# Optimization experiments

Measured on AMD Instinct MI355X. Metric: run time of the kernel, lower is better.

Reference implementation:

```python
import jax, jax.numpy as jnp
import numpy as np

N_NODES = 50000
N_EDGES = 600000
N_RELS = 19
D_IN = 128
D_HID = 64
D_OUT = 2


def setup_inputs() -> dict:
    key = jax.random.key(0)
    ks = jax.random.split(key, 10)
    feat = jax.random.normal(ks[0], (N_NODES, D_IN), dtype=jnp.float32)
    src = jax.random.randint(ks[1], (N_EDGES,), 0, N_NODES)
    dst = jax.random.randint(ks[2], (N_EDGES,), 0, N_NODES)
    etype = jax.random.randint(ks[3], (N_EDGES,), 0, N_RELS)
    s1 = 1.0 / np.sqrt(D_IN)
    s2 = 1.0 / np.sqrt(D_HID)
    W1 = jax.random.normal(ks[4], (N_RELS, D_IN, D_HID), dtype=jnp.float32) * s1
    loop1 = jax.random.normal(ks[5], (D_IN, D_HID), dtype=jnp.float32) * s1
    b1 = jnp.zeros((D_HID,), dtype=jnp.float32)
    W2 = jax.random.normal(ks[6], (N_RELS, D_HID, D_OUT), dtype=jnp.float32) * s2
    loop2 = jax.random.normal(ks[7], (D_HID, D_OUT), dtype=jnp.float32) * s2
    b2 = jnp.zeros((D_OUT,), dtype=jnp.float32)
    return {"feat": feat, "W1": W1, "loop1": loop1, "b1": b1,
            "W2": W2, "loop2": loop2, "b2": b2,
            "src": src, "dst": dst, "etype": etype}


def _rel_graph_conv(h, W, loop_w, bias, src, dst, etype, activation):
    # Per-relation transform of all nodes: [N, R, O]; then gather per edge.
    # (num_rels * out_feat is small, so this is cheaper than gathering W per edge.)
    transformed = jnp.einsum('nd,rdo->nro', h, W)
    msg = transformed[src, etype]                      # [E, O] edge messages
    agg = jax.ops.segment_sum(msg, dst, num_segments=h.shape[0])  # scatter-add
    out = agg + h @ loop_w + bias                      # self-loop + bias
    if activation is not None:
        out = activation(out)
    return out


def reference(feat, W1, loop1, b1, W2, loop2, b2, src, dst, etype):
    h = _rel_graph_conv(feat, W1, loop1, b1, src, dst, etype, jax.nn.relu)
    h = _rel_graph_conv(h, W2, loop2, b2, src, dst, etype, None)
    return h
```

## Files before the change

kernel.cpp:

```cpp
#include <hip/hip_runtime.h>

#define N_NODES 50000
#define N_EDGES 600000
#define N_RELS  19
#define D_IN    128
#define D_HID   64
#define D_OUT   2
#define EDGE_TILES ((N_EDGES + 127) / 128 + N_RELS)
#define SL_BLOCKS  ((N_NODES + 63) / 64)
#define PREP_ELEMS (N_RELS * D_HID * D_IN + 48 * 64 + D_HID * D_IN)
#define PREP_BLOCKS ((PREP_ELEMS + 255) / 256)

typedef unsigned short u16;
typedef unsigned int   u32;
typedef __attribute__((ext_vector_type(8))) short sfrag;
typedef __attribute__((ext_vector_type(4))) float f32x4;

__device__ __forceinline__ u16 f2bf(float f){
  union { float f; u32 i; } v; v.f = f;
  u32 r = v.i + 0x7fffu + ((v.i >> 16) & 1u);
  return (u16)(r >> 16);
}
__device__ __forceinline__ float bf2f(u16 u){
  union { u32 i; float f; } v; v.i = ((u32)u) << 16; return v.f;
}

__global__ __launch_bounds__(256) void k_fused_pre(const float* __restrict__ feat,
                                                   u16* __restrict__ featb,
                                                   const int* __restrict__ et,
                                                   const int* __restrict__ dst,
                                                   int* __restrict__ hist_rel,
                                                   int* __restrict__ hist_dst){
  int i = blockIdx.x * 256 + threadIdx.x;
  float2 f = ((const float2*)feat)[i];
  ((u32*)featb)[i] = (u32)f2bf(f.x) | ((u32)f2bf(f.y) << 16);
  if (blockIdx.x < (N_EDGES + 255) / 256) {
    __shared__ int lh[N_RELS];
    int tid = threadIdx.x;
    if (tid < N_RELS) lh[tid] = 0;
    __syncthreads();
    int e = blockIdx.x * 256 + tid;
    if (e < N_EDGES) {
      atomicAdd(&lh[et[e]], 1);
      atomicAdd(&hist_dst[dst[e]], 1);
    }
    __syncthreads();
    if (tid < N_RELS && lh[tid]) atomicAdd(&hist_rel[tid], lh[tid]);
  }
}

__global__ __launch_bounds__(256) void k_alloc_scan(
    const int* __restrict__ hist_dst, int* __restrict__ dstart,
    int* __restrict__ cur_dst, int* __restrict__ gcnt,
    const int* __restrict__ hist_rel, int* __restrict__ offs,
    int* __restrict__ toff, int* __restrict__ cur_rel,
    const float* __restrict__ W1, const float* __restrict__ loop1,
    const float* __restrict__ W2, u16* __restrict__ W1Tb,
    u16* __restrict__ loop1Tb, u16* __restrict__ W2allT){
  if (blockIdx.x >= 197) {
    int idx = (blockIdx.x - 197) * 256 + threadIdx.x;
    const int T1 = N_RELS * D_HID * D_IN;
    const int T2c = T1 + 48 * 64;
    const int T3 = T2c + D_HID * D_IN;
    if (idx < T1) {
      int r = idx / (D_HID * D_IN);
      int t = idx - r * (D_HID * D_IN);
      int j = t >> 7, d = t & 127;
      W1Tb[idx] = f2bf(W1[(r * D_IN + d) * D_HID + j]);
    } else if (idx < T2c) {
      int k2 = idx - T1;
      int n = k2 >> 6, k = k2 & 63;
      float val = 0.f;
      if (n < N_RELS * D_OUT) {
        int r = n >> 1, o = n & 1;
        val = W2[(r * D_HID + k) * D_OUT + o];
      }
      W2allT[k2] = f2bf(val);
    } else if (idx < T3) {
      int k2 = idx - T2c;
      int j = k2 >> 7, d = k2 & 127;
      loop1Tb[k2] = f2bf(loop1[d * D_HID + j]);
    }
    return;
  }
  if (blockIdx.x == 196) {
    if (threadIdx.x == 0) {
      int acc = 0, tacc = 0;
      offs[0] = 0; toff[0] = 0;
      for (int r = 0; r < N_RELS; ++r) {
        cur_rel[r] = acc;
        int c = hist_rel[r];
        acc += c;                offs[r + 1] = acc;
        tacc += (c + 127) >> 7;  toff[r + 1] = tacc;
      }
    }
    return;
  }
  __shared__ int wbase[4];
  int tid = threadIdx.x, lane = tid & 63, wv = tid >> 6;
  int n = blockIdx.x * 256 + tid;
  int v = (n < N_NODES) ? hist_dst[n] : 0;
  int x = v;
  #pragma unroll
  for (int o = 1; o < 64; o <<= 1) { int u = __shfl_up(x, o); if (lane >= o) x += u; }
  if (lane == 63) wbase[wv] = atomicAdd(gcnt, x);
  __syncthreads();
  int start = wbase[wv] + x - v;
  if (n < N_NODES) { dstart[n] = start; cur_dst[n] = start; }
}

__global__ __launch_bounds__(256) void k_scatter_rel(const int* __restrict__ et,
                                                     int* __restrict__ cursor,
                                                     int* __restrict__ perm){
  __shared__ int lh[N_RELS], base[N_RELS];
  int tid = threadIdx.x;
  if (tid < N_RELS) lh[tid] = 0;
  __syncthreads();
  int e = blockIdx.x * 256 + tid;
  int r = 0, my = 0;
  bool valid = e < N_EDGES;
  if (valid) { r = et[e]; my = atomicAdd(&lh[r], 1); }
  __syncthreads();
  if (tid < N_RELS && lh[tid]) base[tid] = atomicAdd(&cursor[tid], lh[tid]);
  __syncthreads();
  if (valid) perm[base[r] + my] = e;
}

__global__ __launch_bounds__(256) void k_se1(
    const u16* __restrict__ featb, const u16* __restrict__ W1Tb,
    const u16* __restrict__ loop1Tb, const float* __restrict__ b1,
    const int* __restrict__ src, const int* __restrict__ dst,
    const int* __restrict__ perm, const int* __restrict__ offs,
    const int* __restrict__ toff, int* __restrict__ cur_dst,
    u16* __restrict__ msgbuf, float* __restrict__ agg1f){
  __shared__ __align__(16) u16 Bls[64][136];
  __shared__ __align__(16) u16 msg[128][72];
  __shared__ int posIds[128];
  int tid = threadIdx.x, lane = tid & 63, w = tid >> 6;
  int r16 = lane & 15, c4 = lane >> 4;

  if (blockIdx.x >= EDGE_TILES) {
    int base = (blockIdx.x - EDGE_TILES) * 64;
    { int j = tid >> 2, seg = tid & 3;
      const uint4* g = (const uint4*)(loop1Tb + j * 128) + seg * 4;
      uint4* d = (uint4*)&Bls[j][seg * 32];
      d[0] = g[0]; d[1] = g[1]; d[2] = g[2]; d[3] = g[3]; }
    int arow = base + w * 16 + r16; if (arow >= N_NODES) arow = N_NODES - 1;
    sfrag aF[4];
    #pragma unroll
    for (int kk = 0; kk < 4; ++kk)
      aF[kk] = *(const sfrag*)(featb + (size_t)arow * D_IN + kk * 32 + c4 * 8);
    __syncthreads();
    #pragma unroll
    for (int ct = 0; ct < 4; ++ct) {
      f32x4 acc = {0.f, 0.f, 0.f, 0.f};
      #pragma unroll
      for (int kk = 0; kk < 4; ++kk) {
        sfrag bF = *(const sfrag*)&Bls[ct * 16 + r16][kk * 32 + c4 * 8];
        acc = __builtin_amdgcn_mfma_f32_16x16x32_bf16(aF[kk], bF, acc, 0, 0, 0);
      }
      int col = ct * 16 + r16;
      float bias = b1[col];
      #pragma unroll
      for (int reg = 0; reg < 4; ++reg) {
        int orow = base + w * 16 + c4 * 4 + reg;
        if (orow < N_NODES) agg1f[(size_t)orow * D_HID + col] = acc[reg] + bias;
      }
    }
    return;
  }

  int b = blockIdx.x;
  unsigned long long mm = __ballot((lane < N_RELS) && (b >= toff[lane + 1]));
  int rel = __popcll(mm);
  if (rel >= N_RELS) return;
  int ts = offs[rel] + ((b - toff[rel]) << 7);
  int vc = offs[rel + 1] - ts; if (vc > 128) vc = 128;

  int myPos = -1;
  if (tid < 128 && tid < vc) {
    int e = perm[ts + tid];
    myPos = atomicAdd(&cur_dst[dst[e]], 1);
  }
  {
    int j = tid >> 2, seg = tid & 3;
    const uint4* g = (const uint4*)(W1Tb + ((size_t)rel * 64 + j) * 128) + seg * 4;
    uint4* d = (uint4*)&Bls[j][seg * 32];
    d[0] = g[0]; d[1] = g[1]; d[2] = g[2]; d[3] = g[3];
  }
  sfrag aF[2][4];
  #pragma unroll
  for (int mt = 0; mt < 2; ++mt) {
    int row = w * 32 + mt * 16 + r16;
    int rr = row < vc ? row : vc - 1;
    int s = src[perm[ts + rr]];
    const u16* ap = featb + (size_t)s * D_IN + c4 * 8;
    #pragma unroll
    for (int kk = 0; kk < 4; ++kk)
      aF[mt][kk] = *(const sfrag*)(ap + kk * 32);
  }
  __syncthreads();
  #pragma unroll
  for (int ct = 0; ct < 4; ++ct) {
    sfrag bF[4];
    #pragma unroll
    for (int kk = 0; kk < 4; ++kk)
      bF[kk] = *(const sfrag*)&Bls[ct * 16 + r16][kk * 32 + c4 * 8];
    #pragma unroll
    for (int mt = 0; mt < 2; ++mt) {
      f32x4 acc = {0.f, 0.f, 0.f, 0.f};
      #pragma unroll
      for (int kk = 0; kk < 4; ++kk)
        acc = __builtin_amdgcn_mfma_f32_16x16x32_bf16(aF[mt][kk], bF[kk], acc, 0, 0, 0);
      #pragma unroll
      for (int reg = 0; reg < 4; ++reg) {
        float v = acc[reg];
        float o = __shfl_xor(v, 1);
        float lo = (lane & 1) ? o : v;
        float hi = (lane & 1) ? v : o;
        u32 pk = (u32)f2bf(lo) | ((u32)f2bf(hi) << 16);
        if (!(lane & 1)) {
          int orow = w * 32 + mt * 16 + c4 * 4 + reg;
          *(u32*)&msg[orow][ct * 16 + r16] = pk;
        }
      }
    }
  }
  if (tid < 128) posIds[tid] = myPos;
  __syncthreads();
  { int row = tid >> 1, half = tid & 1;
    int pos = posIds[row];
    if (pos >= 0) {
      const uint4* mr = (const uint4*)&msg[row][half * 32];
      uint4* d = (uint4*)(msgbuf + (size_t)pos * D_HID + half * 32);
      d[0] = mr[0]; d[1] = mr[1]; d[2] = mr[2]; d[3] = mr[3];
    } }
}

__global__ __launch_bounds__(256) void k_agg_relu_self2(
    const u16* __restrict__ msgbuf, const int* __restrict__ dstart,
    const int* __restrict__ cnt, const float* __restrict__ agg1f,
    const float* __restrict__ loop2, const float* __restrict__ b2,
    u16* __restrict__ h1b, float* __restrict__ out){
  int wv = threadIdx.x >> 6, lane = threadIdx.x & 63;
  int n = blockIdx.x * 4 + wv;
  int s = dstart[n], epos = s + cnt[n];
  int h = lane >> 5, c = lane & 31;
  float a0 = 0.f, a1 = 0.f;
  for (int i = s + h; i < epos; i += 2) {
    u32 v = ((const u32*)msgbuf)[(size_t)i * 32 + c];
    a0 += bf2f((u16)(v & 0xffffu));
    a1 += bf2f((u16)(v >> 16));
  }
  a0 += __shfl_down(a0, 32);
  a1 += __shfl_down(a1, 32);
  float p0 = 0.f, p1 = 0.f;
  if (h == 0) {
    float2 sl = ((const float2*)(agg1f + (size_t)n * D_HID))[c];
    float v0 = a0 + sl.x, v1 = a1 + sl.y;
    v0 = v0 > 0.f ? v0 : 0.f;
    v1 = v1 > 0.f ? v1 : 0.f;
    ((u32*)h1b)[(size_t)n * 32 + c] = (u32)f2bf(v0) | ((u32)f2bf(v1) << 16);
    float2 w0 = ((const float2*)loop2)[2 * c];
    float2 w1 = ((const float2*)loop2)[2 * c + 1];
    p0 = v0 * w0.x + v1 * w1.x;
    p1 = v0 * w0.y + v1 * w1.y;
  }
  #pragma unroll
  for (int off = 16; off; off >>= 1) {
    p0 += __shfl_down(p0, off);
    p1 += __shfl_down(p1, off);
  }
  if (lane == 0) {
    out[n * 2]     = p0 + b2[0];
    out[n * 2 + 1] = p1 + b2[1];
  }
}

__global__ __launch_bounds__(256) void k_t2(
    const u16* __restrict__ h1b, const u16* __restrict__ W2allT,
    float* __restrict__ T2){
  __shared__ __align__(16) u16 Bls[48][72];
  int tid = threadIdx.x, lane = tid & 63, w = tid >> 6;
  int r16 = lane & 15, c4 = lane >> 4;
  for (int idx = tid; idx < 48 * 8; idx += 256) {
    int row = idx >> 3, q = idx & 7;
    ((uint4*)&Bls[row][0])[q] = ((const uint4*)W2allT)[idx];
  }
  int base = blockIdx.x * 64;
  int arow = base + w * 16 + r16; if (arow >= N_NODES) arow = N_NODES - 1;
  sfrag aF[2];
  #pragma unroll
  for (int kk = 0; kk < 2; ++kk)
    aF[kk] = *(const sfrag*)(h1b + (size_t)arow * D_HID + kk * 32 + c4 * 8);
  __syncthreads();
  #pragma unroll
  for (int ct = 0; ct < 3; ++ct) {
    f32x4 acc = {0.f, 0.f, 0.f, 0.f};
    #pragma unroll
    for (int kk = 0; kk < 2; ++kk) {
      sfrag bF = *(const sfrag*)&Bls[ct * 16 + r16][kk * 32 + c4 * 8];
      acc = __builtin_amdgcn_mfma_f32_16x16x32_bf16(aF[kk], bF, acc, 0, 0, 0);
    }
    int col = ct * 16 + r16;
    if (col < N_RELS * D_OUT) {
      #pragma unroll
      for (int reg = 0; reg < 4; ++reg) {
        int orow = base + w * 16 + c4 * 4 + reg;
        if (orow < N_NODES) T2[(size_t)orow * 40 + col] = acc[reg];
      }
    }
  }
}

__global__ __launch_bounds__(256) void k_edge2(
    const float* __restrict__ T2, const int* __restrict__ src,
    const int* __restrict__ dst, const int* __restrict__ et,
    float* __restrict__ out){
  int e = blockIdx.x * 256 + threadIdx.x;
  if (e >= N_EDGES) return;
  int s = src[e], d = dst[e], r = et[e];
  float2 v = *(const float2*)(T2 + (size_t)s * 40 + r * 2);
  atomicAdd(&out[d * 2],     v.x);
  atomicAdd(&out[d * 2 + 1], v.y);
}

extern "C" void kernel_launch(void* const* d_in, const int* in_sizes, int n_in,
                              void* d_out, int out_size, void* d_ws, size_t ws_size,
                              hipStream_t stream){
  const float* feat  = (const float*)d_in[0];
  const float* W1    = (const float*)d_in[1];
  const float* loop1 = (const float*)d_in[2];
  const float* b1    = (const float*)d_in[3];
  const float* W2    = (const float*)d_in[4];
  const float* loop2 = (const float*)d_in[5];
  const float* b2    = (const float*)d_in[6];
  const int* src     = (const int*)d_in[7];
  const int* dst     = (const int*)d_in[8];
  const int* et      = (const int*)d_in[9];
  float* out = (float*)d_out;

  char* w = (char*)d_ws;
  u16*   W1Tb     = (u16*)(w);
  u16*   W2allT   = (u16*)(w + 311296);
  u16*   loop1Tb  = (u16*)(w + 350208);
  int*   hist_rel = (int*)(w + 366592);
  int*   gcnt     = (int*)(w + 366720);
  int*   hist_dst = (int*)(w + 366848);
  int*   offs     = (int*)(w + 566848);
  int*   toff     = (int*)(w + 566976);
  int*   cur_rel  = (int*)(w + 567104);
  int*   dstart   = (int*)(w + 567232);
  int*   cur_dst  = (int*)(w + 767232);
  int*   perm     = (int*)(w + 967232);
  u16*   featb    = (u16*)(w + 3367232);
  float* T2f      = (float*)(w + 3367232);
  float* agg1f    = (float*)(w + 16167232);
  u16*   h1b      = (u16*)(w + 28967232);
  u16*   msgbuf   = (u16*)(w + 35367232);

  hipMemsetAsync(w + 366592, 0, 200256, stream);
  k_fused_pre     <<<12500, 256, 0, stream>>>(feat, featb, et, dst, hist_rel, hist_dst);
  k_alloc_scan    <<<197 + PREP_BLOCKS, 256, 0, stream>>>(
                      hist_dst, dstart, cur_dst, gcnt, hist_rel, offs, toff, cur_rel,
                      W1, loop1, W2, W1Tb, loop1Tb, W2allT);
  k_scatter_rel   <<<2344,  256, 0, stream>>>(et, cur_rel, perm);
  k_se1           <<<EDGE_TILES + SL_BLOCKS, 256, 0, stream>>>(
                      featb, W1Tb, loop1Tb, b1, src, dst, perm, offs, toff,
                      cur_dst, msgbuf, agg1f);
  k_agg_relu_self2<<<12500, 256, 0, stream>>>(msgbuf, dstart, hist_dst, agg1f,
                                              loop2, b2, h1b, out);
  k_t2            <<<SL_BLOCKS, 256, 0, stream>>>(h1b, W2allT, T2f);
  k_edge2         <<<(N_EDGES + 255) / 256, 256, 0, stream>>>(T2f, src, dst, et, out);
}
```

Measured before the change: 337.8 us.

## Bucket edges by destination block and relation, aggregate in shared memory

Measured after the change: 498.7 us. 1.48x slower.

```diff
diff --git a/kernel.cpp b/kernel.cpp
--- a/kernel.cpp
+++ b/kernel.cpp
@@ -6,9 +6,9 @@
 #define D_IN    128
 #define D_HID   64
 #define D_OUT   2
-#define EDGE_TILES ((N_EDGES + 127) / 128 + N_RELS)
-#define SL_BLOCKS  ((N_NODES + 63) / 64)
-#define PREP_ELEMS (N_RELS * D_HID * D_IN + 48 * 64 + D_HID * D_IN)
+#define NBD     ((N_NODES + 63) >> 6)
+#define NSEG    (NBD * N_RELS)
+#define PREP_ELEMS (N_RELS * D_HID * D_IN + 64 * 64 + D_HID * D_IN)
 #define PREP_BLOCKS ((PREP_ELEMS + 255) / 256)
 
 typedef unsigned short u16;
@@ -21,308 +21,253 @@
   u32 r = v.i + 0x7fffu + ((v.i >> 16) & 1u);
   return (u16)(r >> 16);
 }
-__device__ __forceinline__ float bf2f(u16 u){
-  union { u32 i; float f; } v; v.i = ((u32)u) << 16; return v.f;
-}
-
-__global__ __launch_bounds__(256) void k_fused_pre(const float* __restrict__ feat,
-                                                   u16* __restrict__ featb,
-                                                   const int* __restrict__ et,
-                                                   const int* __restrict__ dst,
-                                                   int* __restrict__ hist_rel,
-                                                   int* __restrict__ hist_dst){
+__device__ __forceinline__ u32 pack2(float lo, float hi){
+  return (u32)f2bf(lo) | ((u32)f2bf(hi) << 16);
+}
+
+__global__ __launch_bounds__(256) void k_pre(const float* __restrict__ feat,
+                                             u16* __restrict__ featb,
+                                             const int* __restrict__ dst,
+                                             const int* __restrict__ et,
+                                             int* __restrict__ seg_hist){
   int i = blockIdx.x * 256 + threadIdx.x;
-  float2 f = ((const float2*)feat)[i];
-  ((u32*)featb)[i] = (u32)f2bf(f.x) | ((u32)f2bf(f.y) << 16);
-  if (blockIdx.x < (N_EDGES + 255) / 256) {
-    __shared__ int lh[N_RELS];
+  float4 f = ((const float4*)feat)[i];
+  uint2 p; p.x = pack2(f.x, f.y); p.y = pack2(f.z, f.w);
+  ((uint2*)featb)[i] = p;
+  if (i < N_EDGES) {
+    int key = (dst[i] >> 6) * N_RELS + et[i];
+    atomicAdd(&seg_hist[key * 4], 1);
+  }
+}
+
+__global__ __launch_bounds__(256) void k_prep(
+    const int* __restrict__ seg_hist, int* __restrict__ seg_off,
+    int* __restrict__ cur_seg,
+    const float* __restrict__ W1, const float* __restrict__ loop1,
+    const float* __restrict__ W2, const float* __restrict__ loop2,
+    u16* __restrict__ W1Tb, u16* __restrict__ loop1Tb,
+    u16* __restrict__ W2allT){
+  if (blockIdx.x == 0) {
+    __shared__ int ps[256];
     int tid = threadIdx.x;
-    if (tid < N_RELS) lh[tid] = 0;
+    const int PER = (NSEG + 255) / 256;
+    int lo = tid * PER, hi = lo + PER; if (hi > NSEG) hi = NSEG; if (lo > NSEG) lo = NSEG;
+    int s = 0;
+    for (int i = lo; i < hi; ++i) s += seg_hist[i * 4];
+    ps[tid] = s;
     __syncthreads();
-    int e = blockIdx.x * 256 + tid;
-    if (e < N_EDGES) {
-      atomicAdd(&lh[et[e]], 1);
-      atomicAdd(&hist_dst[dst[e]], 1);
-    }
+    if (tid == 0) { int a = 0; for (int j = 0; j < 256; ++j) { int x = ps[j]; ps[j] = a; a += x; } }
     __syncthreads();
-    if (tid < N_RELS && lh[tid]) atomicAdd(&hist_rel[tid], lh[tid]);
-  }
-}
-
-__global__ __launch_bounds__(256) void k_alloc_scan(
-    const int* __restrict__ hist_dst, int* __restrict__ dstart,
-    int* __restrict__ cur_dst, int* __restrict__ gcnt,
-    const int* __restrict__ hist_rel, int* __restrict__ offs,
-    int* __restrict__ toff, int* __restrict__ cur_rel,
-    const float* __restrict__ W1, const float* __restrict__ loop1,
-    const float* __restrict__ W2, u16* __restrict__ W1Tb,
-    u16* __restrict__ loop1Tb, u16* __restrict__ W2allT){
-  if (blockIdx.x >= 197) {
-    int idx = (blockIdx.x - 197) * 256 + threadIdx.x;
-    const int T1 = N_RELS * D_HID * D_IN;
-    const int T2c = T1 + 48 * 64;
-    const int T3 = T2c + D_HID * D_IN;
-    if (idx < T1) {
-      int r = idx / (D_HID * D_IN);
-      int t = idx - r * (D_HID * D_IN);
-      int j = t >> 7, d = t & 127;
-      W1Tb[idx] = f2bf(W1[(r * D_IN + d) * D_HID + j]);
-    } else if (idx < T2c) {
-      int k2 = idx - T1;
-      int n = k2 >> 6, k = k2 & 63;
-      float val = 0.f;
-      if (n < N_RELS * D_OUT) {
-        int r = n >> 1, o = n & 1;
-        val = W2[(r * D_HID + k) * D_OUT + o];
-      }
-      W2allT[k2] = f2bf(val);
-    } else if (idx < T3) {
-      int k2 = idx - T2c;
-      int j = k2 >> 7, d = k2 & 127;
-      loop1Tb[k2] = f2bf(loop1[d * D_HID + j]);
-    }
+    int eo = ps[tid];
+    for (int i = lo; i < hi; ++i) {
+      int c = seg_hist[i * 4];
+      seg_off[i] = eo; cur_seg[i * 4] = eo;
+      eo += c;
+    }
+    if (hi == NSEG) seg_off[NSEG] = eo;
     return;
   }
-  if (blockIdx.x == 196) {
-    if (threadIdx.x == 0) {
-      int acc = 0, tacc = 0;
-      offs[0] = 0; toff[0] = 0;
-      for (int r = 0; r < N_RELS; ++r) {
-        cur_rel[r] = acc;
-        int c = hist_rel[r];
-        acc += c;                offs[r + 1] = acc;
-        tacc += (c + 127) >> 7;  toff[r + 1] = tacc;
-      }
-    }
-    return;
-  }
-  __shared__ int wbase[4];
-  int tid = threadIdx.x, lane = tid & 63, wv = tid >> 6;
-  int n = blockIdx.x * 256 + tid;
-  int v = (n < N_NODES) ? hist_dst[n] : 0;
-  int x = v;
-  #pragma unroll
-  for (int o = 1; o < 64; o <<= 1) { int u = __shfl_up(x, o); if (lane >= o) x += u; }
-  if (lane == 63) wbase[wv] = atomicAdd(gcnt, x);
-  __syncthreads();
-  int start = wbase[wv] + x - v;
-  if (n < N_NODES) { dstart[n] = start; cur_dst[n] = start; }
-}
-
-__global__ __launch_bounds__(256) void k_scatter_rel(const int* __restrict__ et,
-                                                     int* __restrict__ cursor,
-                                                     int* __restrict__ perm){
-  __shared__ int lh[N_RELS], base[N_RELS];
-  int tid = threadIdx.x;
-  if (tid < N_RELS) lh[tid] = 0;
-  __syncthreads();
-  int e = blockIdx.x * 256 + tid;
-  int r = 0, my = 0;
-  bool valid = e < N_EDGES;
-  if (valid) { r = et[e]; my = atomicAdd(&lh[r], 1); }
-  __syncthreads();
-  if (tid < N_RELS && lh[tid]) base[tid] = atomicAdd(&cursor[tid], lh[tid]);
-  __syncthreads();
-  if (valid) perm[base[r] + my] = e;
-}
-
-__global__ __launch_bounds__(256) void k_se1(
+  int idx = (blockIdx.x - 1) * 256 + threadIdx.x;
+  const int T1  = N_RELS * D_HID * D_IN;
+  const int T2c = T1 + 64 * 64;
+  const int T3  = T2c + D_HID * D_IN;
+  if (idx < T1) {
+    int r = idx / (D_HID * D_IN);
+    int t = idx - r * (D_HID * D_IN);
+    int j = t >> 7, d = t & 127;
+    W1Tb[idx] = f2bf(W1[(r * D_IN + d) * D_HID + j]);
+  } else if (idx < T2c) {
+    int k2 = idx - T1;
+    int j = k2 >> 6, k = k2 & 63;
+    float val = 0.f;
+    if (j < N_RELS * D_OUT)      val = W2[((j >> 1) * D_HID + k) * D_OUT + (j & 1)];
+    else if (j == 38)            val = loop2[k * 2];
+    else if (j == 39)            val = loop2[k * 2 + 1];
+    W2allT[k2] = f2bf(val);
+  } else if (idx < T3) {
+    int k2 = idx - T2c;
+    int j = k2 >> 7, d = k2 & 127;
+    loop1Tb[k2] = f2bf(loop1[d * D_HID + j]);
+  }
+}
+
+__global__ __launch_bounds__(256) void k_scatter(const int* __restrict__ dst,
+                                                 const int* __restrict__ et,
+                                                 int* __restrict__ cur_seg,
+                                                 int* __restrict__ perm){
+  int e = blockIdx.x * 256 + threadIdx.x;
+  if (e >= N_EDGES) return;
+  int key = (dst[e] >> 6) * N_RELS + et[e];
+  int p = atomicAdd(&cur_seg[key * 4], 1);
+  perm[p] = e;
+}
+
+__global__ __launch_bounds__(256, 4) void k_edge1(
     const u16* __restrict__ featb, const u16* __restrict__ W1Tb,
-    const u16* __restrict__ loop1Tb, const float* __restrict__ b1,
     const int* __restrict__ src, const int* __restrict__ dst,
-    const int* __restrict__ perm, const int* __restrict__ offs,
-    const int* __restrict__ toff, int* __restrict__ cur_dst,
-    u16* __restrict__ msgbuf, float* __restrict__ agg1f){
-  __shared__ __align__(16) u16 Bls[64][136];
-  __shared__ __align__(16) u16 msg[128][72];
-  __shared__ int posIds[128];
+    const int* __restrict__ perm, const int* __restrict__ seg_off,
+    float* __restrict__ agg1f){
+  __shared__ float agg[64][68];
+  __shared__ int wdl[256];
   int tid = threadIdx.x, lane = tid & 63, w = tid >> 6;
   int r16 = lane & 15, c4 = lane >> 4;
-
-  if (blockIdx.x >= EDGE_TILES) {
-    int base = (blockIdx.x - EDGE_TILES) * 64;
-    { int j = tid >> 2, seg = tid & 3;
-      const uint4* g = (const uint4*)(loop1Tb + j * 128) + seg * 4;
-      uint4* d = (uint4*)&Bls[j][seg * 32];
-      d[0] = g[0]; d[1] = g[1]; d[2] = g[2]; d[3] = g[3]; }
-    int arow = base + w * 16 + r16; if (arow >= N_NODES) arow = N_NODES - 1;
-    sfrag aF[4];
-    #pragma unroll
-    for (int kk = 0; kk < 4; ++kk)
-      aF[kk] = *(const sfrag*)(featb + (size_t)arow * D_IN + kk * 32 + c4 * 8);
-    __syncthreads();
-    #pragma unroll
-    for (int ct = 0; ct < 4; ++ct) {
-      f32x4 acc = {0.f, 0.f, 0.f, 0.f};
+  int kb = blockIdx.x;
+  for (int i = tid; i < 64 * 68; i += 256) (&agg[0][0])[i] = 0.f;
+  __syncthreads();
+
+  int tcnt = 0;
+  int sb = kb * N_RELS;
+  int sPrev = seg_off[sb];
+  for (int rel = 0; rel < N_RELS; ++rel) {
+    int s0 = sPrev, s1 = seg_off[sb + rel + 1];
+    sPrev = s1;
+    int c = s1 - s0;
+    int nt = (c + 63) >> 6;
+    const u16* bp = W1Tb + (size_t)rel * (D_HID * D_IN);
+    for (int t = 0; t < nt; ++t, ++tcnt) {
+      if ((tcnt & 3) != w) continue;
+      int ts = s0 + (t << 6);
+      int vc = c - (t << 6); if (vc > 64) vc = 64;
+      sfrag aF[4][4];
       #pragma unroll
-      for (int kk = 0; kk < 4; ++kk) {
-        sfrag bF = *(const sfrag*)&Bls[ct * 16 + r16][kk * 32 + c4 * 8];
-        acc = __builtin_amdgcn_mfma_f32_16x16x32_bf16(aF[kk], bF, acc, 0, 0, 0);
+      for (int mt = 0; mt < 4; ++mt) {
+        int row = mt * 16 + r16;
+        int rr = row < vc ? row : vc - 1;
+        int e = perm[ts + rr];
+        if (c4 == 0) wdl[w * 64 + row] = (row < vc) ? (dst[e] & 63) : -1;
+        const u16* ap = featb + (size_t)src[e] * D_IN + c4 * 8;
+        #pragma unroll
+        for (int kk = 0; kk < 4; ++kk)
+          aF[mt][kk] = *(const sfrag*)(ap + kk * 32);
       }
-      int col = ct * 16 + r16;
-      float bias = b1[col];
       #pragma unroll
-      for (int reg = 0; reg < 4; ++reg) {
-        int orow = base + w * 16 + c4 * 4 + reg;
-        if (orow < N_NODES) agg1f[(size_t)orow * D_HID + col] = acc[reg] + bias;
+      for (int ct = 0; ct < 4; ++ct) {
+        int col = ct * 16 + r16;
+        sfrag bF[4];
+        #pragma unroll
+        for (int kk = 0; kk < 4; ++kk)
+          bF[kk] = *(const sfrag*)(bp + (size_t)col * D_IN + kk * 32 + c4 * 8);
+        #pragma unroll
+        for (int mt = 0; mt < 4; ++mt) {
+          f32x4 acc = {0.f, 0.f, 0.f, 0.f};
+          #pragma unroll
+          for (int kk = 0; kk < 4; ++kk)
+            acc = __builtin_amdgcn_mfma_f32_16x16x32_bf16(aF[mt][kk], bF[kk], acc, 0, 0, 0);
+          int4 dlq = *((const int4*)&wdl[w * 64 + mt * 16 + c4 * 4]);
+          int dls[4] = {dlq.x, dlq.y, dlq.z, dlq.w};
+          #pragma unroll
+          for (int reg = 0; reg < 4; ++reg)
+            if (dls[reg] >= 0) atomicAdd(&agg[dls[reg]][col], acc[reg]);
+        }
       }
     }
-    return;
-  }
-
-  int b = blockIdx.x;
-  unsigned long long mm = __ballot((lane < N_RELS) && (b >= toff[lane + 1]));
-  int rel = __popcll(mm);
-  if (rel >= N_RELS) return;
-  int ts = offs[rel] + ((b - toff[rel]) << 7);
-  int vc = offs[rel + 1] - ts; if (vc > 128) vc = 128;
-
-  int myPos = -1;
-  if (tid < 128 && tid < vc) {
-    int e = perm[ts + tid];
-    myPos = atomicAdd(&cur_dst[dst[e]], 1);
-  }
-  {
-    int j = tid >> 2, seg = tid & 3;
-    const uint4* g = (const uint4*)(W1Tb + ((size_t)rel * 64 + j) * 128) + seg * 4;
-    uint4* d = (uint4*)&Bls[j][seg * 32];
-    d[0] = g[0]; d[1] = g[1]; d[2] = g[2]; d[3] = g[3];
-  }
-  sfrag aF[2][4];
+  }
+  __syncthreads();
+  { int row = tid >> 2, q = tid & 3;
+    int n = kb * 64 + row;
+    if (n < N_NODES) {
+      float4* d = (float4*)(agg1f + (size_t)n * D_HID + q * 16);
+      const float4* s4 = (const float4*)&agg[row][q * 16];
+      d[0] = s4[0]; d[1] = s4[1]; d[2] = s4[2]; d[3] = s4[3];
+    } }
+}
+
+__global__ __launch_bounds__(256) void k_post(
+    const u16* __restrict__ featb, const u16* __restrict__ loop1Tb,
+    const float* __restrict__ b1, const float* __restrict__ agg1f,
+    const u16* __restrict__ W2allT, const float* __restrict__ b2,
+    float* __restrict__ T2f, float* __restrict__ out){
+  __shared__ __align__(16) u16 Bls[64][136];
+  __shared__ __align__(16) u16 msg[64][72];
+  int tid = threadIdx.x, lane = tid & 63, w = tid >> 6;
+  int r16 = lane & 15, c4 = lane >> 4;
+  int base = blockIdx.x * 64;
+  { int j = tid >> 2, sg = tid & 3;
+    const uint4* g = (const uint4*)(loop1Tb + j * 128) + sg * 4;
+    uint4* d = (uint4*)&Bls[j][sg * 32];
+    d[0] = g[0]; d[1] = g[1]; d[2] = g[2]; d[3] = g[3]; }
+  int arow = base + w * 16 + r16; if (arow >= N_NODES) arow = N_NODES - 1;
+  sfrag aF[4];
   #pragma unroll
-  for (int mt = 0; mt < 2; ++mt) {
-    int row = w * 32 + mt * 16 + r16;
-    int rr = row < vc ? row : vc - 1;
-    int s = src[perm[ts + rr]];
-    const u16* ap = featb + (size_t)s * D_IN + c4 * 8;
-    #pragma unroll
-    for (int kk = 0; kk < 4; ++kk)
-      aF[mt][kk] = *(const sfrag*)(ap + kk * 32);
-  }
+  for (int kk = 0; kk < 4; ++kk)
+    aF[kk] = *(const sfrag*)(featb + (size_t)arow * D_IN + kk * 32 + c4 * 8);
   __syncthreads();
   #pragma unroll
   for (int ct = 0; ct < 4; ++ct) {
-    sfrag bF[4];
+    f32x4 acc = {0.f, 0.f, 0.f, 0.f};
     #pragma unroll
-    for (int kk = 0; kk < 4; ++kk)
-      bF[kk] = *(const sfrag*)&Bls[ct * 16 + r16][kk * 32 + c4 * 8];
+    for (int kk = 0; kk < 4; ++kk) {
+      sfrag bF = *(const sfrag*)&Bls[ct * 16 + r16][kk * 32 + c4 * 8];
+      acc = __builtin_amdgcn_mfma_f32_16x16x32_bf16(aF[kk], bF, acc, 0, 0, 0);
+    }
+    int col = ct * 16 + r16;
+    float bias = b1[col];
     #pragma unroll
-    for (int mt = 0; mt < 2; ++mt) {
-      f32x4 acc = {0.f, 0.f, 0.f, 0.f};
-      #pragma unroll
-      for (int kk = 0; kk < 4; ++kk)
-        acc = __builtin_amdgcn_mfma_f32_16x16x32_bf16(aF[mt][kk], bF[kk], acc, 0, 0, 0);
-      #pragma unroll
-      for (int reg = 0; reg < 4; ++reg) {
-        float v = acc[reg];
-        float o = __shfl_xor(v, 1);
-        float lo = (lane & 1) ? o : v;
-        float hi = (lane & 1) ? v : o;
-        u32 pk = (u32)f2bf(lo) | ((u32)f2bf(hi) << 16);
-        if (!(lane & 1)) {
-          int orow = w * 32 + mt * 16 + c4 * 4 + reg;
-          *(u32*)&msg[orow][ct * 16 + r16] = pk;
-        }
-      }
-    }
-  }
-  if (tid < 128) posIds[tid] = myPos;
-  __syncthreads();
-  { int row = tid >> 1, half = tid & 1;
-    int pos = posIds[row];
-    if (pos >= 0) {
-      const uint4* mr = (const uint4*)&msg[row][half * 32];
-      uint4* d = (uint4*)(msgbuf + (size_t)pos * D_HID + half * 32);
-      d[0] = mr[0]; d[1] = mr[1]; d[2] = mr[2]; d[3] = mr[3];
-    } }
-}
-
-__global__ __launch_bounds__(256) void k_agg_relu_self2(
-    const u16* __restrict__ msgbuf, const int* __restrict__ dstart,
-    const int* __restrict__ cnt, const float* __restrict__ agg1f,
-    const float* __restrict__ loop2, const float* __restrict__ b2,
-    u16* __restrict__ h1b, float* __restrict__ out){
-  int wv = threadIdx.x >> 6, lane = threadIdx.x & 63;
-  int n = blockIdx.x * 4 + wv;
-  int s = dstart[n], epos = s + cnt[n];
-  int h = lane >> 5, c = lane & 31;
-  float a0 = 0.f, a1 = 0.f;
-  for (int i = s + h; i < epos; i += 2) {
-    u32 v = ((const u32*)msgbuf)[(size_t)i * 32 + c];
-    a0 += bf2f((u16)(v & 0xffffu));
-    a1 += bf2f((u16)(v >> 16));
-  }
-  a0 += __shfl_down(a0, 32);
-  a1 += __shfl_down(a1, 32);
-  float p0 = 0.f, p1 = 0.f;
-  if (h == 0) {
-    float2 sl = ((const float2*)(agg1f + (size_t)n * D_HID))[c];
-    float v0 = a0 + sl.x, v1 = a1 + sl.y;
-    v0 = v0 > 0.f ? v0 : 0.f;
-    v1 = v1 > 0.f ? v1 : 0.f;
-    ((u32*)h1b)[(size_t)n * 32 + c] = (u32)f2bf(v0) | ((u32)f2bf(v1) << 16);
-    float2 w0 = ((const float2*)loop2)[2 * c];
-    float2 w1 = ((const float2*)loop2)[2 * c + 1];
-    p0 = v0 * w0.x + v1 * w1.x;
-    p1 = v0 * w0.y + v1 * w1.y;
-  }
-  #pragma unroll
-  for (int off = 16; off; off >>= 1) {
-    p0 += __shfl_down(p0, off);
-    p1 += __shfl_down(p1, off);
-  }
-  if (lane == 0) {
-    out[n * 2]     = p0 + b2[0];
-    out[n * 2 + 1] = p1 + b2[1];
-  }
-}
-
-__global__ __launch_bounds__(256) void k_t2(
-    const u16* __restrict__ h1b, const u16* __restrict__ W2allT,
-    float* __restrict__ T2){
-  __shared__ __align__(16) u16 Bls[48][72];
-  int tid = threadIdx.x, lane = tid & 63, w = tid >> 6;
-  int r16 = lane & 15, c4 = lane >> 4;
-  for (int idx = tid; idx < 48 * 8; idx += 256) {
-    int row = idx >> 3, q = idx & 7;
-    ((uint4*)&Bls[row][0])[q] = ((const uint4*)W2allT)[idx];
-  }
-  int base = blockIdx.x * 64;
-  int arow = base + w * 16 + r16; if (arow >= N_NODES) arow = N_NODES - 1;
-  sfrag aF[2];
+    for (int reg = 0; reg < 4; ++reg) {
+      int row = w * 16 + c4 * 4 + reg;
+      int n = base + row;
+      float m = (n < N_NODES) ? agg1f[(size_t)n * D_HID + col] : 0.f;
+      float v = acc[reg] + m + bias;
+      v = v > 0.f ? v : 0.f;
+      float o = __shfl_xor(v, 1);
+      if (!(lane & 1))
+        *(u32*)&msg[row][col] = pack2(v, o);
+    }
+  }
+  __syncthreads();
+  { int rw = tid >> 2, q = tid & 3;
+    uint4* d = (uint4*)&Bls[rw][0];
+    const uint4* g = (const uint4*)(W2allT + rw * 64);
+    d[q * 2] = g[q * 2]; d[q * 2 + 1] = g[q * 2 + 1]; }
+  __syncthreads();
+  sfrag aM[2];
   #pragma unroll
   for (int kk = 0; kk < 2; ++kk)
-    aF[kk] = *(const sfrag*)(h1b + (size_t)arow * D_HID + kk * 32 + c4 * 8);
-  __syncthreads();
+    aM[kk] = *(const sfrag*)&msg[w * 16 + r16][kk * 32 + c4 * 8];
   #pragma unroll
   for (int ct = 0; ct < 3; ++ct) {
+    int col = ct * 16 + r16;
     f32x4 acc = {0.f, 0.f, 0.f, 0.f};
     #pragma unroll
     for (int kk = 0; kk < 2; ++kk) {
-      sfrag bF = *(const sfrag*)&Bls[ct * 16 + r16][kk * 32 + c4 * 8];
-      acc = __builtin_amdgcn_mfma_f32_16x16x32_bf16(aF[kk], bF, acc, 0, 0, 0);
-    }
-    int col = ct * 16 + r16;
-    if (col < N_RELS * D_OUT) {
-      #pragma unroll
-      for (int reg = 0; reg < 4; ++reg) {
-        int orow = base + w * 16 + c4 * 4 + reg;
-        if (orow < N_NODES) T2[(size_t)orow * 40 + col] = acc[reg];
+      sfrag bF = *(const sfrag*)&Bls[col][kk * 32 + c4 * 8];
+      acc = __builtin_amdgcn_mfma_f32_16x16x32_bf16(aM[kk], bF, acc, 0, 0, 0);
+    }
+    #pragma unroll
+    for (int reg = 0; reg < 4; ++reg) {
+      int n = base + w * 16 + c4 * 4 + reg;
+      if (n < N_NODES) {
+        if (col < 38)        T2f[(size_t)n * 40 + col] = acc[reg];
+        else if (col < 40)   out[n * 2 + (col - 38)] = acc[reg] + b2[col - 38];
       }
     }
   }
 }
 
-__global__ __launch_bounds__(256) void k_edge2(
-    const float* __restrict__ T2, const int* __restrict__ src,
-    const int* __restrict__ dst, const int* __restrict__ et,
+__global__ __launch_bounds__(256) void k_fin(
+    const float* __restrict__ T2f, const int* __restrict__ perm,
+    const int* __restrict__ src, const int* __restrict__ dst,
+    const int* __restrict__ et, const int* __restrict__ seg_off,
     float* __restrict__ out){
-  int e = blockIdx.x * 256 + threadIdx.x;
-  if (e >= N_EDGES) return;
-  int s = src[e], d = dst[e], r = et[e];
-  float2 v = *(const float2*)(T2 + (size_t)s * 40 + r * 2);
-  atomicAdd(&out[d * 2],     v.x);
-  atomicAdd(&out[d * 2 + 1], v.y);
+  __shared__ float a2[64][2];
+  int tid = threadIdx.x;
+  int kb = blockIdx.x;
+  if (tid < 128) (&a2[0][0])[tid] = 0.f;
+  __syncthreads();
+  int e0 = seg_off[kb * N_RELS], e1 = seg_off[kb * N_RELS + N_RELS];
+  for (int p = e0 + tid; p < e1; p += 256) {
+    int e = perm[p];
+    float2 v = *(const float2*)(T2f + (size_t)src[e] * 40 + et[e] * 2);
+    int dl = dst[e] & 63;
+    atomicAdd(&a2[dl][0], v.x);
+    atomicAdd(&a2[dl][1], v.y);
+  }
+  __syncthreads();
+  if (tid < 128) {
+    int row = tid >> 1, q = tid & 1;
+    int n = kb * 64 + row;
+    if (n < N_NODES) out[n * 2 + q] += a2[row][q];
+  }
 }
 
 extern "C" void kernel_launch(void* const* d_in, const int* in_sizes, int n_in,
@@ -343,33 +288,22 @@
   char* w = (char*)d_ws;
   u16*   W1Tb     = (u16*)(w);
   u16*   W2allT   = (u16*)(w + 311296);
-  u16*   loop1Tb  = (u16*)(w + 350208);
-  int*   hist_rel = (int*)(w + 366592);
-  int*   gcnt     = (int*)(w + 366720);
-  int*   hist_dst = (int*)(w + 366848);
-  int*   offs     = (int*)(w + 566848);
-  int*   toff     = (int*)(w + 566976);
-  int*   cur_rel  = (int*)(w + 567104);
-  int*   dstart   = (int*)(w + 567232);
-  int*   cur_dst  = (int*)(w + 767232);
-  int*   perm     = (int*)(w + 967232);
-  u16*   featb    = (u16*)(w + 3367232);
-  float* T2f      = (float*)(w + 3367232);
-  float* agg1f    = (float*)(w + 16167232);
-  u16*   h1b      = (u16*)(w + 28967232);
-  u16*   msgbuf   = (u16*)(w + 35367232);
-
-  hipMemsetAsync(w + 366592, 0, 200256, stream);
-  k_fused_pre     <<<12500, 256, 0, stream>>>(feat, featb, et, dst, hist_rel, hist_dst);
-  k_alloc_scan    <<<197 + PREP_BLOCKS, 256, 0, stream>>>(
-                      hist_dst, dstart, cur_dst, gcnt, hist_rel, offs, toff, cur_rel,
-                      W1, loop1, W2, W1Tb, loop1Tb, W2allT);
-  k_scatter_rel   <<<2344,  256, 0, stream>>>(et, cur_rel, perm);
-  k_se1           <<<EDGE_TILES + SL_BLOCKS, 256, 0, stream>>>(
-                      featb, W1Tb, loop1Tb, b1, src, dst, perm, offs, toff,
-                      cur_dst, msgbuf, agg1f);
-  k_agg_relu_self2<<<12500, 256, 0, stream>>>(msgbuf, dstart, hist_dst, agg1f,
-                                              loop2, b2, h1b, out);
-  k_t2            <<<SL_BLOCKS, 256, 0, stream>>>(h1b, W2allT, T2f);
-  k_edge2         <<<(N_EDGES + 255) / 256, 256, 0, stream>>>(T2f, src, dst, et, out);
-}
+  u16*   loop1Tb  = (u16*)(w + 319488);
+  int*   seg_hist = (int*)(w + 335872);
+  int*   seg_off  = (int*)(w + 573600);
+  int*   cur_seg  = (int*)(w + 633040);
+  int*   perm     = (int*)(w + 870768);
+  u16*   featb    = (u16*)(w + 3270768);
+  float* agg1f    = (float*)(w + 16070768);
+  float* T2f      = (float*)(w + 28883056);
+
+  hipMemsetAsync(w + 335872, 0, 237728, stream);
+  k_pre     <<<6250, 256, 0, stream>>>(feat, featb, dst, et, seg_hist);
+  k_prep    <<<1 + PREP_BLOCKS, 256, 0, stream>>>(seg_hist, seg_off, cur_seg,
+                                                  W1, loop1, W2, loop2,
+                                                  W1Tb, loop1Tb, W2allT);
+  k_scatter <<<2344, 256, 0, stream>>>(dst, et, cur_seg, perm);
+  k_edge1   <<<NBD, 256, 0, stream>>>(featb, W1Tb, src, dst, perm, seg_off, agg1f);
+  k_post    <<<NBD, 256, 0, stream>>>(featb, loop1Tb, b1, agg1f, W2allT, b2, T2f, out);
+  k_fin     <<<NBD, 256, 0, stream>>>(T2f, perm, src, dst, et, seg_off, out);
+}
```
